# Kernel tuning notes

Measured on AMD Instinct MI355X. Metric: run time of the kernel, lower is better.

Reference implementation:

```python
import jax, jax.numpy as jnp
import numpy as np

D = 1024      # d_model
H = 16        # n_heads
HD = D // H   # head_dim = 64
B = 2
T = 2048


def setup_inputs() -> dict:
    key = jax.random.key(0)
    k0, k1, k2 = jax.random.split(key, 3)
    s = 1.0 / np.sqrt(D)
    return {
        "x": jax.random.normal(k0, (B, T, D), dtype=jnp.float32),
        "qkv_w": jax.random.normal(k1, (D, 3 * D), dtype=jnp.float32) * s,
        "qkv_b": jnp.zeros((3 * D,), dtype=jnp.float32),
        "out_w": jax.random.normal(k2, (D, D), dtype=jnp.float32) * s,
        "out_b": jnp.zeros((D,), dtype=jnp.float32),
    }


def _apply_rotary(x, rope):
    # Faithful to the torch apply_rotary: even/odd interleaved split of both
    # x and the [sin(freqs)|cos(freqs)] rope table.
    x1, x2 = x[..., ::2], x[..., 1::2]
    sin, cos = rope[..., ::2], rope[..., 1::2]
    return jnp.concatenate([x1 * cos - x2 * sin, x1 * sin + x2 * cos], axis=-1)


def reference(x, qkv_w, qkv_b, out_w, out_b):
    Bx, Tx, Dm = x.shape
    # QKV projection -> [3, B, H, T, HD]
    qkv = (x @ qkv_w + qkv_b).reshape(Bx, Tx, 3, H, HD).transpose(2, 0, 3, 1, 4)
    q, k, v = qkv[0], qkv[1], qkv[2]

    # Rotary table: rope = concat(sin(freqs), cos(freqs)) along last dim -> [T, HD]
    inv_freq = 1.0 / (10000.0 ** (jnp.arange(0, HD, 2, dtype=jnp.float32) / HD))
    t = jnp.arange(Tx, dtype=jnp.float32)
    freqs = t[:, None] * inv_freq[None, :]          # [T, HD/2]
    rope = jnp.concatenate([jnp.sin(freqs), jnp.cos(freqs)], axis=-1)  # [T, HD]

    q = _apply_rotary(q, rope)
    k = _apply_rotary(k, rope)

    scale = HD ** -0.5
    scores = jnp.einsum('bhqd,bhkd->bhqk', q, k) * scale  # [B,H,T,T]
    causal_mask = jnp.triu(jnp.ones((Tx, Tx), dtype=bool), 1)
    scores = jnp.where(causal_mask, -jnp.inf, scores)
    attn = jax.nn.softmax(scores, axis=-1)
    # dropout is identity in eval mode
    out = jnp.einsum('bhqk,bhkd->bhqd', attn, v)           # [B,H,T,HD]
    out = out.transpose(0, 2, 1, 3).reshape(Bx, Tx, Dm)    # [B,T,D]
    return out @ out_w + out_b
```

## Files before the change

### kernel.cpp

```cpp
#include <hip/hip_runtime.h>

typedef unsigned short u16;
typedef __attribute__((ext_vector_type(8))) __bf16 bf16x8;
typedef __attribute__((ext_vector_type(4))) float f32x4;

#define NB 2
#define NT 2048
#define ND 1024
#define NH 16
#define HD 64

__device__ __forceinline__ float b2f(u16 u) {
  union { float f; unsigned int i; } v; v.i = ((unsigned int)u) << 16; return v.f;
}
__device__ __forceinline__ u16 f2b(float f) {
  union { float f; unsigned int i; } v; v.f = f;
  unsigned int r = (v.i + 0x7FFFu + ((v.i >> 16) & 1u)) >> 16;
  return (u16)r;
}

__device__ __forceinline__ void gload_lds16(const u16* g, u16* lds) {
  __builtin_amdgcn_global_load_lds(
      (const __attribute__((address_space(1))) unsigned int*)(g),
      (__attribute__((address_space(3))) unsigned int*)(lds),
      16, 0, 0);
}

__device__ __forceinline__ f32x4 mfma16(bf16x8 a, bf16x8 b, f32x4 c) {
  return __builtin_amdgcn_mfma_f32_16x16x32_bf16(a, b, c, 0, 0, 0);
}

template <int N>
__device__ __forceinline__ float ror16(float x) {
  return __int_as_float(__builtin_amdgcn_update_dpp(
      __float_as_int(x), __float_as_int(x), 0x120 | N, 0xF, 0xF, true));
}
__device__ __forceinline__ float rsum16(float x) {
  x += ror16<8>(x);
  x += ror16<4>(x);
  x += ror16<2>(x);
  x += ror16<1>(x);
  return x;
}

__device__ __forceinline__ float fast_sin(float a) {
  float r = a * 0.15915494309189535f;
  r -= floorf(r);
  return __builtin_amdgcn_sinf(r);
}
__device__ __forceinline__ float fast_cos(float a) {
  float r = a * 0.15915494309189535f;
  r -= floorf(r);
  return __builtin_amdgcn_cosf(r);
}

__global__ __launch_bounds__(256) void cast_f32_bf16(const float* __restrict__ in,
                                                     u16* __restrict__ out, int n) {
  int i = (blockIdx.x * 256 + threadIdx.x) * 8;
  if (i + 8 <= n) {
#pragma unroll
    for (int j = 0; j < 8; ++j) out[i + j] = f2b(in[i + j]);
  }
}

__global__ __launch_bounds__(256) void transpose_cast(const float* __restrict__ in,
                                                      u16* __restrict__ out,
                                                      int K, int N) {
  __shared__ u16 tile[32][33];
  int n0 = blockIdx.x * 32, k0 = blockIdx.y * 32;
  int tx = threadIdx.x, ty = threadIdx.y;
  for (int i = ty; i < 32; i += 8)
    tile[i][tx] = f2b(in[(size_t)(k0 + i) * N + n0 + tx]);
  __syncthreads();
  for (int i = ty; i < 32; i += 8)
    out[(size_t)(n0 + i) * K + k0 + tx] = tile[tx][i];
}

template <int BM, bool F32OUT>
__global__ __launch_bounds__(256) void gemm_bt(const u16* __restrict__ A,
                                               const u16* __restrict__ Bt,
                                               const float* __restrict__ bias,
                                               void* __restrict__ Cv,
                                               int M, int N, int K) {
  constexpr int MI = BM / 32;
  __shared__ alignas(16) u16 As[BM * 32];
  __shared__ alignas(16) u16 Bs[128 * 32];
  const int tid = threadIdx.x;
  const int lane = tid & 63;
  const int wave = tid >> 6;
  const int l15 = lane & 15, quad = lane >> 4;
  const int wm = (wave >> 1) * (BM / 2), wn = (wave & 1) * 64;
  const int row0 = blockIdx.y * BM, col0 = blockIdx.x * 128;

  f32x4 acc[MI][4] = {};

  for (int k0 = 0; k0 < K; k0 += 32) {
    __syncthreads();
#pragma unroll
    for (int p = 0; p < BM / 64; ++p) {
      int idx8 = p * 256 + tid;
      int r = idx8 >> 2, c = (idx8 & 3) * 8;
      gload_lds16(&A[(size_t)(row0 + r) * K + k0 + c], &As[idx8 * 8]);
    }
#pragma unroll
    for (int p = 0; p < 2; ++p) {
      int idx8 = p * 256 + tid;
      int r = idx8 >> 2, c = (idx8 & 3) * 8;
      gload_lds16(&Bt[(size_t)(col0 + r) * K + k0 + c], &Bs[idx8 * 8]);
    }
    __syncthreads();
    bf16x8 af[MI], bfr[4];
#pragma unroll
    for (int mi = 0; mi < MI; ++mi)
      af[mi] = *(const bf16x8*)&As[(wm + mi * 16 + l15) * 32 + quad * 8];
#pragma unroll
    for (int ni = 0; ni < 4; ++ni)
      bfr[ni] = *(const bf16x8*)&Bs[(wn + ni * 16 + l15) * 32 + quad * 8];
#pragma unroll
    for (int mi = 0; mi < MI; ++mi)
#pragma unroll
      for (int ni = 0; ni < 4; ++ni)
        acc[mi][ni] = mfma16(af[mi], bfr[ni], acc[mi][ni]);
  }

#pragma unroll
  for (int ni = 0; ni < 4; ++ni) {
    int c = col0 + wn + ni * 16 + l15;
    float bv = bias[c];
#pragma unroll
    for (int mi = 0; mi < MI; ++mi) {
      int r0 = row0 + wm + mi * 16 + quad * 4;
      f32x4 v = acc[mi][ni];
#pragma unroll
      for (int r = 0; r < 4; ++r) {
        if (F32OUT)
          ((float*)Cv)[(size_t)(r0 + r) * N + c] = v[r] + bv;
        else
          ((u16*)Cv)[(size_t)(r0 + r) * N + c] = f2b(v[r] + bv);
      }
    }
  }
}

__global__ __launch_bounds__(256) void rope_frag(const u16* __restrict__ qkv,
                                                 u16* __restrict__ qsw,
                                                 u16* __restrict__ ksw) {
  __shared__ u16 tq[32 * 72];
  __shared__ u16 tk[32 * 72];
  const int bh = blockIdx.y;
  const int b = bh >> 4, h = bh & 15;
  const int t0 = blockIdx.x * 32;
  const int tid = threadIdx.x;

  {
    int row = tid >> 3, col = (tid & 7) * 8;
    const u16* src = &qkv[(size_t)(b * NT + t0 + row) * 3072 + h * HD + col];
    *(bf16x8*)&tq[row * 72 + col] = *(const bf16x8*)src;
    *(bf16x8*)&tk[row * 72 + col] = *(const bf16x8*)(src + ND);
  }
  __syncthreads();

  const int isK = tid >> 7;
  const int chunk = (tid >> 4) & 7;
  const int tl = tid & 15;
  const int ks = chunk >> 2, quad = chunk & 3;
  const u16* tile = isK ? tk : tq;
  u16* dst = isK ? ksw : qsw;
  const float scale = isK ? 1.0f : 0.125f;
  const float LOG1E4 = 9.210340371976184f;

#pragma unroll
  for (int rbloc = 0; rbloc < 2; ++rbloc) {
    const int row = rbloc * 16 + tl;
    const float tf = (float)(t0 + row);
    union { u16 s[8]; bf16x8 v; } o;
#pragma unroll
    for (int e = 0; e < 8; ++e) {
      int c = ks * 32 + quad * 8 + e;
      int j = c & 31;
      int c1 = 2 * j, c2 = 2 * j + 1;
      float inv1 = __expf(-((float)(c1 & 31)) * (1.0f / 32.0f) * LOG1E4);
      float inv2 = __expf(-((float)(c2 & 31)) * (1.0f / 32.0f) * LOG1E4);
      float a1 = tf * inv1, a2 = tf * inv2;
      float sA = (c1 < 32) ? fast_sin(a1) : fast_cos(a1);
      float cA = (c2 < 32) ? fast_sin(a2) : fast_cos(a2);
      float x1 = b2f(tile[row * 72 + c1]), x2 = b2f(tile[row * 72 + c2]);
      float ov = (c < 32) ? (x1 * cA - x2 * sA) : (x1 * sA + x2 * cA);
      o.s[e] = f2b(ov * scale);
    }
    size_t addr =
        ((((size_t)bh * 128 + (t0 >> 4) + rbloc) * 2 + ks) * 64 + quad * 16 + tl) * 8;
    *(bf16x8*)&dst[addr] = o.v;
  }
}

__global__ __launch_bounds__(256) void vtrans_frag(const u16* __restrict__ qkv,
                                                   u16* __restrict__ vsw) {
  __shared__ u16 tv[32 * 72];
  const int bh = blockIdx.y;
  const int b = bh >> 4, h = bh & 15;
  const int kb = blockIdx.x;
  const int tid = threadIdx.x;
  {
    int row = tid >> 3, col = (tid & 7) * 8;
    *(bf16x8*)&tv[row * 72 + col] = *(const bf16x8*)&qkv[
        (size_t)(b * NT + kb * 32 + row) * 3072 + 2 * ND + h * HD + col];
  }
  __syncthreads();
  const int ni = tid >> 6, lane = tid & 63;
  const int quad = lane >> 4, l15 = lane & 15;
  union { u16 s[8]; bf16x8 v; } o;
#pragma unroll
  for (int e = 0; e < 8; ++e)
    o.s[e] = tv[(quad * 8 + e) * 72 + ni * 16 + l15];
  *(bf16x8*)&vsw[(((size_t)bh * 64 + kb) * 4 + ni) * 512 + lane * 8] = o.v;
}

__global__ __launch_bounds__(128, 3) void flash_kernel(const u16* __restrict__ qsw,
                                                       const u16* __restrict__ ksw,
                                                       const u16* __restrict__ vsw,
                                                       u16* __restrict__ attn) {
  __shared__ alignas(16) u16 Ps[2 * 5120];
  __shared__ float Ll[32];

  const int tid = threadIdx.x;
  const int w = tid >> 6;
  const int lane = tid & 63;
  const int l15 = lane & 15, quad = lane >> 4;
  const int linear = (int)blockIdx.x;
  const int bh = linear & 31;
  const int qt = 63 - (linear >> 5);
  const int r0 = qt * 32;
  u16* Psw = &Ps[w * 5120];

  bf16x8 aq[2][2];
#pragma unroll
  for (int mi = 0; mi < 2; ++mi)
#pragma unroll
    for (int ks = 0; ks < 2; ++ks)
      aq[mi][ks] = *(const bf16x8*)&qsw[
          ((((size_t)bh * 128 + qt * 2 + mi) * 2 + ks) * 64 + lane) * 8];

  f32x4 oacc[2][4] = {};
  float lst[8] = {0.f, 0.f, 0.f, 0.f, 0.f, 0.f, 0.f, 0.f};

  const int ktmax = qt >> 2;
  for (int kt = w; kt <= ktmax; kt += 2) {
    f32x4 sacc[2][8] = {};
#pragma unroll
    for (int ks = 0; ks < 2; ++ks)
#pragma unroll
      for (int ni = 0; ni < 8; ++ni) {
        bf16x8 kf = *(const bf16x8*)&ksw[
            ((((size_t)bh * 128 + kt * 8 + ni) * 2 + ks) * 64 + lane) * 8];
        sacc[0][ni] = mfma16(aq[0][ks], kf, sacc[0][ni]);
        sacc[1][ni] = mfma16(aq[1][ks], kf, sacc[1][ni]);
      }

    const bool diag = (kt == ktmax);
    const int k0 = kt * 128;
#pragma unroll
    for (int mi = 0; mi < 2; ++mi)
#pragma unroll
      for (int r = 0; r < 4; ++r) {
        const int prow = mi * 16 + quad * 4 + r;
        float sv[8];
#pragma unroll
        for (int ni = 0; ni < 8; ++ni) sv[ni] = sacc[mi][ni][r];
        if (diag) {
#pragma unroll
          for (int ni = 0; ni < 8; ++ni)
            if (k0 + ni * 16 + l15 > r0 + prow) sv[ni] = -__builtin_inff();
        }
        float rs = 0.f;
#pragma unroll
        for (int ni = 0; ni < 8; ++ni) {
          float p = __expf(sv[ni]);
          sv[ni] = p;
          rs += p;
        }
        lst[mi * 4 + r] += rsum16(rs);
#pragma unroll
        for (int ni = 0; ni < 8; ++ni)
          Psw[(ni >> 1) * 1280 + prow * 40 + (ni & 1) * 16 + l15] = f2b(sv[ni]);
      }

    asm volatile("" ::: "memory");

#pragma unroll
    for (int ks = 0; ks < 4; ++ks) {
      bf16x8 vf[4];
#pragma unroll
      for (int ni = 0; ni < 4; ++ni)
        vf[ni] = *(const bf16x8*)&vsw[
            (((size_t)bh * 64 + kt * 4 + ks) * 4 + ni) * 512 + lane * 8];
      bf16x8 ap0 = *(const bf16x8*)&Psw[ks * 1280 + l15 * 40 + quad * 8];
      bf16x8 ap1 = *(const bf16x8*)&Psw[ks * 1280 + (16 + l15) * 40 + quad * 8];
#pragma unroll
      for (int ni = 0; ni < 4; ++ni) {
        oacc[0][ni] = mfma16(ap0, vf[ni], oacc[0][ni]);
        oacc[1][ni] = mfma16(ap1, vf[ni], oacc[1][ni]);
      }
    }
  }

  float* Of = (float*)&Ps[5120];
  if (w == 1) {
#pragma unroll
    for (int mi = 0; mi < 2; ++mi)
#pragma unroll
      for (int r = 0; r < 4; ++r) {
        const int row = mi * 16 + quad * 4 + r;
        if (l15 == 0) Ll[row] = lst[mi * 4 + r];
#pragma unroll
        for (int ni = 0; ni < 4; ++ni)
          Of[row * 64 + ni * 16 + l15] = oacc[mi][ni][r];
      }
  }
  __syncthreads();
  if (w == 0) {
    const int b = bh >> 4, h = bh & 15;
#pragma unroll
    for (int mi = 0; mi < 2; ++mi)
#pragma unroll
      for (int r = 0; r < 4; ++r) {
        const int row = mi * 16 + quad * 4 + r;
        const float rl = 1.0f / (lst[mi * 4 + r] + Ll[row]);
        const int trow = r0 + row;
#pragma unroll
        for (int ni = 0; ni < 4; ++ni) {
          float o = oacc[mi][ni][r] + Of[row * 64 + ni * 16 + l15];
          attn[((size_t)b * NT + trow) * ND + h * HD + ni * 16 + l15] = f2b(o * rl);
        }
      }
  }
}

extern "C" void kernel_launch(void* const* d_in, const int* in_sizes, int n_in,
                              void* d_out, int out_size, void* d_ws, size_t ws_size,
                              hipStream_t stream) {
  const float* x = (const float*)d_in[0];
  const float* qkv_w = (const float*)d_in[1];
  const float* qkv_b = (const float*)d_in[2];
  const float* out_w = (const float*)d_in[3];
  const float* out_b = (const float*)d_in[4];
  float* out = (float*)d_out;

  u16* ws = (u16*)d_ws;
  u16* xb    = ws;
  u16* wqkvT = xb + (size_t)4096 * 1024;
  u16* woutT = wqkvT + 3072 * 1024;
  u16* qkv   = woutT + 1024 * 1024;
  u16* qsw   = qkv + (size_t)4096 * 3072;
  u16* ksw   = qsw + (size_t)32 * 2048 * 64;
  u16* vsw   = ksw + (size_t)32 * 2048 * 64;
  u16* attn  = vsw + (size_t)32 * 2048 * 64;

  cast_f32_bf16<<<(NB * NT * ND) / (256 * 8), 256, 0, stream>>>(
      x, xb, NB * NT * ND);

  transpose_cast<<<dim3(3 * ND / 32, ND / 32), dim3(32, 8), 0, stream>>>(
      qkv_w, wqkvT, ND, 3 * ND);
  transpose_cast<<<dim3(ND / 32, ND / 32), dim3(32, 8), 0, stream>>>(
      out_w, woutT, ND, ND);

  gemm_bt<128, false><<<dim3(3 * ND / 128, NB * NT / 128), 256, 0, stream>>>(
      xb, wqkvT, qkv_b, qkv, NB * NT, 3 * ND, ND);

  rope_frag<<<dim3(NT / 32, NB * NH), 256, 0, stream>>>(qkv, qsw, ksw);
  vtrans_frag<<<dim3(NT / 32, NB * NH), 256, 0, stream>>>(qkv, vsw);

  flash_kernel<<<dim3(2048), 128, 0, stream>>>(qsw, ksw, vsw, attn);

  gemm_bt<64, true><<<dim3(ND / 128, NB * NT / 64), 256, 0, stream>>>(
      attn, woutT, out_b, out, NB * NT, ND, ND);
}
```

Baseline: 207.8 us.

## Fuse V transpose into rope prep, compute row sums via MFMA with exp2

Merges the rope and V-fragment kernels into one launch that loads Q, K and V tiles together. In the flash kernel, log2(e) is folded into the Q scale so exp2f can replace __expf. P is truncated to bf16 instead of rounded. The per-row softmax denominator is now accumulated by an extra MFMA of P against a ones vector, replacing the DPP cross-lane reductions. This trades some VALU and shuffle work for extra MFMA issue. Truncating P and summing the bf16 values slightly changes numerics.

```diff
diff --git a/kernel.cpp b/kernel.cpp
--- a/kernel.cpp
+++ b/kernel.cpp
@@ -28,19 +28,6 @@
 
 __device__ __forceinline__ f32x4 mfma16(bf16x8 a, bf16x8 b, f32x4 c) {
   return __builtin_amdgcn_mfma_f32_16x16x32_bf16(a, b, c, 0, 0, 0);
-}
-
-template <int N>
-__device__ __forceinline__ float ror16(float x) {
-  return __int_as_float(__builtin_amdgcn_update_dpp(
-      __float_as_int(x), __float_as_int(x), 0x120 | N, 0xF, 0xF, true));
-}
-__device__ __forceinline__ float rsum16(float x) {
-  x += ror16<8>(x);
-  x += ror16<4>(x);
-  x += ror16<2>(x);
-  x += ror16<1>(x);
-  return x;
 }
 
 __device__ __forceinline__ float fast_sin(float a) {
@@ -142,11 +129,13 @@
   }
 }
 
-__global__ __launch_bounds__(256) void rope_frag(const u16* __restrict__ qkv,
+__global__ __launch_bounds__(256) void prep_frag(const u16* __restrict__ qkv,
                                                  u16* __restrict__ qsw,
-                                                 u16* __restrict__ ksw) {
+                                                 u16* __restrict__ ksw,
+                                                 u16* __restrict__ vsw) {
   __shared__ u16 tq[32 * 72];
   __shared__ u16 tk[32 * 72];
+  __shared__ u16 tv[32 * 72];
   const int bh = blockIdx.y;
   const int b = bh >> 4, h = bh & 15;
   const int t0 = blockIdx.x * 32;
@@ -157,63 +146,54 @@
     const u16* src = &qkv[(size_t)(b * NT + t0 + row) * 3072 + h * HD + col];
     *(bf16x8*)&tq[row * 72 + col] = *(const bf16x8*)src;
     *(bf16x8*)&tk[row * 72 + col] = *(const bf16x8*)(src + ND);
+    *(bf16x8*)&tv[row * 72 + col] = *(const bf16x8*)(src + 2 * ND);
   }
   __syncthreads();
 
-  const int isK = tid >> 7;
-  const int chunk = (tid >> 4) & 7;
-  const int tl = tid & 15;
-  const int ks = chunk >> 2, quad = chunk & 3;
-  const u16* tile = isK ? tk : tq;
-  u16* dst = isK ? ksw : qsw;
-  const float scale = isK ? 1.0f : 0.125f;
-  const float LOG1E4 = 9.210340371976184f;
-
-#pragma unroll
-  for (int rbloc = 0; rbloc < 2; ++rbloc) {
-    const int row = rbloc * 16 + tl;
-    const float tf = (float)(t0 + row);
+  {
+    const int isK = tid >> 7;
+    const int chunk = (tid >> 4) & 7;
+    const int tl = tid & 15;
+    const int ks = chunk >> 2, quad = chunk & 3;
+    const u16* tile = isK ? tk : tq;
+    u16* dst = isK ? ksw : qsw;
+    const float scale = isK ? 1.0f : 0.18033688011112042f;
+    const float LOG1E4 = 9.210340371976184f;
+
+#pragma unroll
+    for (int rbloc = 0; rbloc < 2; ++rbloc) {
+      const int row = rbloc * 16 + tl;
+      const float tf = (float)(t0 + row);
+      union { u16 s[8]; bf16x8 v; } o;
+#pragma unroll
+      for (int e = 0; e < 8; ++e) {
+        int c = ks * 32 + quad * 8 + e;
+        int j = c & 31;
+        int c1 = 2 * j, c2 = 2 * j + 1;
+        float inv1 = __expf(-((float)(c1 & 31)) * (1.0f / 32.0f) * LOG1E4);
+        float inv2 = __expf(-((float)(c2 & 31)) * (1.0f / 32.0f) * LOG1E4);
+        float a1 = tf * inv1, a2 = tf * inv2;
+        float sA = (c1 < 32) ? fast_sin(a1) : fast_cos(a1);
+        float cA = (c2 < 32) ? fast_sin(a2) : fast_cos(a2);
+        float x1 = b2f(tile[row * 72 + c1]), x2 = b2f(tile[row * 72 + c2]);
+        float ov = (c < 32) ? (x1 * cA - x2 * sA) : (x1 * sA + x2 * cA);
+        o.s[e] = f2b(ov * scale);
+      }
+      size_t addr =
+          ((((size_t)bh * 128 + (t0 >> 4) + rbloc) * 2 + ks) * 64 + quad * 16 + tl) * 8;
+      *(bf16x8*)&dst[addr] = o.v;
+    }
+  }
+
+  {
+    const int ni = tid >> 6, lane = tid & 63;
+    const int quad = lane >> 4, l15 = lane & 15;
     union { u16 s[8]; bf16x8 v; } o;
 #pragma unroll
-    for (int e = 0; e < 8; ++e) {
-      int c = ks * 32 + quad * 8 + e;
-      int j = c & 31;
-      int c1 = 2 * j, c2 = 2 * j + 1;
-      float inv1 = __expf(-((float)(c1 & 31)) * (1.0f / 32.0f) * LOG1E4);
-      float inv2 = __expf(-((float)(c2 & 31)) * (1.0f / 32.0f) * LOG1E4);
-      float a1 = tf * inv1, a2 = tf * inv2;
-      float sA = (c1 < 32) ? fast_sin(a1) : fast_cos(a1);
-      float cA = (c2 < 32) ? fast_sin(a2) : fast_cos(a2);
-      float x1 = b2f(tile[row * 72 + c1]), x2 = b2f(tile[row * 72 + c2]);
-      float ov = (c < 32) ? (x1 * cA - x2 * sA) : (x1 * sA + x2 * cA);
-      o.s[e] = f2b(ov * scale);
-    }
-    size_t addr =
-        ((((size_t)bh * 128 + (t0 >> 4) + rbloc) * 2 + ks) * 64 + quad * 16 + tl) * 8;
-    *(bf16x8*)&dst[addr] = o.v;
-  }
-}
-
-__global__ __launch_bounds__(256) void vtrans_frag(const u16* __restrict__ qkv,
-                                                   u16* __restrict__ vsw) {
-  __shared__ u16 tv[32 * 72];
-  const int bh = blockIdx.y;
-  const int b = bh >> 4, h = bh & 15;
-  const int kb = blockIdx.x;
-  const int tid = threadIdx.x;
-  {
-    int row = tid >> 3, col = (tid & 7) * 8;
-    *(bf16x8*)&tv[row * 72 + col] = *(const bf16x8*)&qkv[
-        (size_t)(b * NT + kb * 32 + row) * 3072 + 2 * ND + h * HD + col];
-  }
-  __syncthreads();
-  const int ni = tid >> 6, lane = tid & 63;
-  const int quad = lane >> 4, l15 = lane & 15;
-  union { u16 s[8]; bf16x8 v; } o;
-#pragma unroll
-  for (int e = 0; e < 8; ++e)
-    o.s[e] = tv[(quad * 8 + e) * 72 + ni * 16 + l15];
-  *(bf16x8*)&vsw[(((size_t)bh * 64 + kb) * 4 + ni) * 512 + lane * 8] = o.v;
+    for (int e = 0; e < 8; ++e)
+      o.s[e] = tv[(quad * 8 + e) * 72 + ni * 16 + l15];
+    *(bf16x8*)&vsw[(((size_t)bh * 64 + (t0 >> 5)) * 4 + ni) * 512 + lane * 8] = o.v;
+  }
 }
 
 __global__ __launch_bounds__(128, 3) void flash_kernel(const u16* __restrict__ qsw,
@@ -233,6 +213,11 @@
   const int r0 = qt * 32;
   u16* Psw = &Ps[w * 5120];
 
+  union { u16 s[8]; bf16x8 v; } onesu;
+#pragma unroll
+  for (int e = 0; e < 8; ++e) onesu.s[e] = 0x3F80;
+  const bf16x8 ones = onesu.v;
+
   bf16x8 aq[2][2];
 #pragma unroll
   for (int mi = 0; mi < 2; ++mi)
@@ -242,7 +227,7 @@
           ((((size_t)bh * 128 + qt * 2 + mi) * 2 + ks) * 64 + lane) * 8];
 
   f32x4 oacc[2][4] = {};
-  float lst[8] = {0.f, 0.f, 0.f, 0.f, 0.f, 0.f, 0.f, 0.f};
+  f32x4 lacc[2] = {};
 
   const int ktmax = qt >> 2;
   for (int kt = w; kt <= ktmax; kt += 2) {
@@ -264,25 +249,14 @@
 #pragma unroll
       for (int r = 0; r < 4; ++r) {
         const int prow = mi * 16 + quad * 4 + r;
-        float sv[8];
-#pragma unroll
-        for (int ni = 0; ni < 8; ++ni) sv[ni] = sacc[mi][ni][r];
-        if (diag) {
-#pragma unroll
-          for (int ni = 0; ni < 8; ++ni)
-            if (k0 + ni * 16 + l15 > r0 + prow) sv[ni] = -__builtin_inff();
+#pragma unroll
+        for (int ni = 0; ni < 8; ++ni) {
+          float s = sacc[mi][ni][r];
+          if (diag && (k0 + ni * 16 + l15 > r0 + prow)) s = -__builtin_inff();
+          float p = exp2f(s);
+          Psw[(ni >> 1) * 1280 + prow * 40 + (ni & 1) * 16 + l15] =
+              (u16)(__float_as_uint(p) >> 16);
         }
-        float rs = 0.f;
-#pragma unroll
-        for (int ni = 0; ni < 8; ++ni) {
-          float p = __expf(sv[ni]);
-          sv[ni] = p;
-          rs += p;
-        }
-        lst[mi * 4 + r] += rsum16(rs);
-#pragma unroll
-        for (int ni = 0; ni < 8; ++ni)
-          Psw[(ni >> 1) * 1280 + prow * 40 + (ni & 1) * 16 + l15] = f2b(sv[ni]);
       }
 
     asm volatile("" ::: "memory");
@@ -301,6 +275,8 @@
         oacc[0][ni] = mfma16(ap0, vf[ni], oacc[0][ni]);
         oacc[1][ni] = mfma16(ap1, vf[ni], oacc[1][ni]);
       }
+      lacc[0] = mfma16(ap0, ones, lacc[0]);
+      lacc[1] = mfma16(ap1, ones, lacc[1]);
     }
   }
 
@@ -311,7 +287,7 @@
 #pragma unroll
       for (int r = 0; r < 4; ++r) {
         const int row = mi * 16 + quad * 4 + r;
-        if (l15 == 0) Ll[row] = lst[mi * 4 + r];
+        if (l15 == 0) Ll[row] = lacc[mi][r];
 #pragma unroll
         for (int ni = 0; ni < 4; ++ni)
           Of[row * 64 + ni * 16 + l15] = oacc[mi][ni][r];
@@ -325,7 +301,7 @@
 #pragma unroll
       for (int r = 0; r < 4; ++r) {
         const int row = mi * 16 + quad * 4 + r;
-        const float rl = 1.0f / (lst[mi * 4 + r] + Ll[row]);
+        const float rl = 1.0f / (lacc[mi][r] + Ll[row]);
         const int trow = r0 + row;
 #pragma unroll
         for (int ni = 0; ni < 4; ++ni) {
@@ -367,8 +343,7 @@
   gemm_bt<128, false><<<dim3(3 * ND / 128, NB * NT / 128), 256, 0, stream>>>(
       xb, wqkvT, qkv_b, qkv, NB * NT, 3 * ND, ND);
 
-  rope_frag<<<dim3(NT / 32, NB * NH), 256, 0, stream>>>(qkv, qsw, ksw);
-  vtrans_frag<<<dim3(NT / 32, NB * NH), 256, 0, stream>>>(qkv, vsw);
+  prep_frag<<<dim3(NT / 32, NB * NH), 256, 0, stream>>>(qkv, qsw, ksw, vsw);
 
   flash_kernel<<<dim3(2048), 128, 0, stream>>>(qsw, ksw, vsw, attn);
 
```

Measured after the change: 211.7 us. About the same (+1.9%).

## Fuse rope and V-transpose kernels; prefetch K/V fragments before softmax in flash loop

Applied to the files above, without the earlier changes.

Merges the rope and V fragment-transpose kernels into one launch that reads the Q, K and V tiles together, removing one kernel launch and a second pass over the qkv buffer. In the flash attention loop, all K fragments for a tile are loaded up front before the QK MFMAs, and all V fragments are issued before the softmax so their global-load latency overlaps the exp/reduction work. The cost is much higher register pressure (16+16 bf16x8 fragments live at once), which may lower occupancy under the launch bound of 3 blocks per CU or cause spills.

```diff
diff --git a/kernel.cpp b/kernel.cpp
--- a/kernel.cpp
+++ b/kernel.cpp
@@ -142,11 +142,13 @@
   }
 }
 
-__global__ __launch_bounds__(256) void rope_frag(const u16* __restrict__ qkv,
+__global__ __launch_bounds__(256) void prep_frag(const u16* __restrict__ qkv,
                                                  u16* __restrict__ qsw,
-                                                 u16* __restrict__ ksw) {
+                                                 u16* __restrict__ ksw,
+                                                 u16* __restrict__ vsw) {
   __shared__ u16 tq[32 * 72];
   __shared__ u16 tk[32 * 72];
+  __shared__ u16 tv[32 * 72];
   const int bh = blockIdx.y;
   const int b = bh >> 4, h = bh & 15;
   const int t0 = blockIdx.x * 32;
@@ -157,63 +159,54 @@
     const u16* src = &qkv[(size_t)(b * NT + t0 + row) * 3072 + h * HD + col];
     *(bf16x8*)&tq[row * 72 + col] = *(const bf16x8*)src;
     *(bf16x8*)&tk[row * 72 + col] = *(const bf16x8*)(src + ND);
+    *(bf16x8*)&tv[row * 72 + col] = *(const bf16x8*)(src + 2 * ND);
   }
   __syncthreads();
 
-  const int isK = tid >> 7;
-  const int chunk = (tid >> 4) & 7;
-  const int tl = tid & 15;
-  const int ks = chunk >> 2, quad = chunk & 3;
-  const u16* tile = isK ? tk : tq;
-  u16* dst = isK ? ksw : qsw;
-  const float scale = isK ? 1.0f : 0.125f;
-  const float LOG1E4 = 9.210340371976184f;
-
-#pragma unroll
-  for (int rbloc = 0; rbloc < 2; ++rbloc) {
-    const int row = rbloc * 16 + tl;
-    const float tf = (float)(t0 + row);
+  {
+    const int isK = tid >> 7;
+    const int chunk = (tid >> 4) & 7;
+    const int tl = tid & 15;
+    const int ks = chunk >> 2, quad = chunk & 3;
+    const u16* tile = isK ? tk : tq;
+    u16* dst = isK ? ksw : qsw;
+    const float scale = isK ? 1.0f : 0.125f;
+    const float LOG1E4 = 9.210340371976184f;
+
+#pragma unroll
+    for (int rbloc = 0; rbloc < 2; ++rbloc) {
+      const int row = rbloc * 16 + tl;
+      const float tf = (float)(t0 + row);
+      union { u16 s[8]; bf16x8 v; } o;
+#pragma unroll
+      for (int e = 0; e < 8; ++e) {
+        int c = ks * 32 + quad * 8 + e;
+        int j = c & 31;
+        int c1 = 2 * j, c2 = 2 * j + 1;
+        float inv1 = __expf(-((float)(c1 & 31)) * (1.0f / 32.0f) * LOG1E4);
+        float inv2 = __expf(-((float)(c2 & 31)) * (1.0f / 32.0f) * LOG1E4);
+        float a1 = tf * inv1, a2 = tf * inv2;
+        float sA = (c1 < 32) ? fast_sin(a1) : fast_cos(a1);
+        float cA = (c2 < 32) ? fast_sin(a2) : fast_cos(a2);
+        float x1 = b2f(tile[row * 72 + c1]), x2 = b2f(tile[row * 72 + c2]);
+        float ov = (c < 32) ? (x1 * cA - x2 * sA) : (x1 * sA + x2 * cA);
+        o.s[e] = f2b(ov * scale);
+      }
+      size_t addr =
+          ((((size_t)bh * 128 + (t0 >> 4) + rbloc) * 2 + ks) * 64 + quad * 16 + tl) * 8;
+      *(bf16x8*)&dst[addr] = o.v;
+    }
+  }
+
+  {
+    const int ni = tid >> 6, lane = tid & 63;
+    const int quad = lane >> 4, l15 = lane & 15;
     union { u16 s[8]; bf16x8 v; } o;
 #pragma unroll
-    for (int e = 0; e < 8; ++e) {
-      int c = ks * 32 + quad * 8 + e;
-      int j = c & 31;
-      int c1 = 2 * j, c2 = 2 * j + 1;
-      float inv1 = __expf(-((float)(c1 & 31)) * (1.0f / 32.0f) * LOG1E4);
-      float inv2 = __expf(-((float)(c2 & 31)) * (1.0f / 32.0f) * LOG1E4);
-      float a1 = tf * inv1, a2 = tf * inv2;
-      float sA = (c1 < 32) ? fast_sin(a1) : fast_cos(a1);
-      float cA = (c2 < 32) ? fast_sin(a2) : fast_cos(a2);
-      float x1 = b2f(tile[row * 72 + c1]), x2 = b2f(tile[row * 72 + c2]);
-      float ov = (c < 32) ? (x1 * cA - x2 * sA) : (x1 * sA + x2 * cA);
-      o.s[e] = f2b(ov * scale);
-    }
-    size_t addr =
-        ((((size_t)bh * 128 + (t0 >> 4) + rbloc) * 2 + ks) * 64 + quad * 16 + tl) * 8;
-    *(bf16x8*)&dst[addr] = o.v;
-  }
-}
-
-__global__ __launch_bounds__(256) void vtrans_frag(const u16* __restrict__ qkv,
-                                                   u16* __restrict__ vsw) {
-  __shared__ u16 tv[32 * 72];
-  const int bh = blockIdx.y;
-  const int b = bh >> 4, h = bh & 15;
-  const int kb = blockIdx.x;
-  const int tid = threadIdx.x;
-  {
-    int row = tid >> 3, col = (tid & 7) * 8;
-    *(bf16x8*)&tv[row * 72 + col] = *(const bf16x8*)&qkv[
-        (size_t)(b * NT + kb * 32 + row) * 3072 + 2 * ND + h * HD + col];
-  }
-  __syncthreads();
-  const int ni = tid >> 6, lane = tid & 63;
-  const int quad = lane >> 4, l15 = lane & 15;
-  union { u16 s[8]; bf16x8 v; } o;
-#pragma unroll
-  for (int e = 0; e < 8; ++e)
-    o.s[e] = tv[(quad * 8 + e) * 72 + ni * 16 + l15];
-  *(bf16x8*)&vsw[(((size_t)bh * 64 + kb) * 4 + ni) * 512 + lane * 8] = o.v;
+    for (int e = 0; e < 8; ++e)
+      o.s[e] = tv[(quad * 8 + e) * 72 + ni * 16 + l15];
+    *(bf16x8*)&vsw[(((size_t)bh * 64 + (t0 >> 5)) * 4 + ni) * 512 + lane * 8] = o.v;
+  }
 }
 
 __global__ __launch_bounds__(128, 3) void flash_kernel(const u16* __restrict__ qsw,
@@ -246,16 +239,30 @@
 
   const int ktmax = qt >> 2;
   for (int kt = w; kt <= ktmax; kt += 2) {
+    bf16x8 kf[2][8];
+#pragma unroll
+    for (int ks = 0; ks < 2; ++ks)
+#pragma unroll
+      for (int ni = 0; ni < 8; ++ni)
+        kf[ks][ni] = *(const bf16x8*)&ksw[
+            ((((size_t)bh * 128 + kt * 8 + ni) * 2 + ks) * 64 + lane) * 8];
+
     f32x4 sacc[2][8] = {};
 #pragma unroll
     for (int ks = 0; ks < 2; ++ks)
 #pragma unroll
       for (int ni = 0; ni < 8; ++ni) {
-        bf16x8 kf = *(const bf16x8*)&ksw[
-            ((((size_t)bh * 128 + kt * 8 + ni) * 2 + ks) * 64 + lane) * 8];
-        sacc[0][ni] = mfma16(aq[0][ks], kf, sacc[0][ni]);
-        sacc[1][ni] = mfma16(aq[1][ks], kf, sacc[1][ni]);
-      }
+        sacc[0][ni] = mfma16(aq[0][ks], kf[ks][ni], sacc[0][ni]);
+        sacc[1][ni] = mfma16(aq[1][ks], kf[ks][ni], sacc[1][ni]);
+      }
+
+    bf16x8 vf[4][4];
+#pragma unroll
+    for (int ks = 0; ks < 4; ++ks)
+#pragma unroll
+      for (int ni = 0; ni < 4; ++ni)
+        vf[ks][ni] = *(const bf16x8*)&vsw[
+            (((size_t)bh * 64 + kt * 4 + ks) * 4 + ni) * 512 + lane * 8];
 
     const bool diag = (kt == ktmax);
     const int k0 = kt * 128;
@@ -289,17 +296,12 @@
 
 #pragma unroll
     for (int ks = 0; ks < 4; ++ks) {
-      bf16x8 vf[4];
-#pragma unroll
-      for (int ni = 0; ni < 4; ++ni)
-        vf[ni] = *(const bf16x8*)&vsw[
-            (((size_t)bh * 64 + kt * 4 + ks) * 4 + ni) * 512 + lane * 8];
       bf16x8 ap0 = *(const bf16x8*)&Psw[ks * 1280 + l15 * 40 + quad * 8];
       bf16x8 ap1 = *(const bf16x8*)&Psw[ks * 1280 + (16 + l15) * 40 + quad * 8];
 #pragma unroll
       for (int ni = 0; ni < 4; ++ni) {
-        oacc[0][ni] = mfma16(ap0, vf[ni], oacc[0][ni]);
-        oacc[1][ni] = mfma16(ap1, vf[ni], oacc[1][ni]);
+        oacc[0][ni] = mfma16(ap0, vf[ks][ni], oacc[0][ni]);
+        oacc[1][ni] = mfma16(ap1, vf[ks][ni], oacc[1][ni]);
       }
     }
   }
@@ -367,8 +369,7 @@
   gemm_bt<128, false><<<dim3(3 * ND / 128, NB * NT / 128), 256, 0, stream>>>(
       xb, wqkvT, qkv_b, qkv, NB * NT, 3 * ND, ND);
 
-  rope_frag<<<dim3(NT / 32, NB * NH), 256, 0, stream>>>(qkv, qsw, ksw);
-  vtrans_frag<<<dim3(NT / 32, NB * NH), 256, 0, stream>>>(qkv, vsw);
+  prep_frag<<<dim3(NT / 32, NB * NH), 256, 0, stream>>>(qkv, qsw, ksw, vsw);
 
   flash_kernel<<<dim3(2048), 128, 0, stream>>>(qsw, ksw, vsw, attn);
 
```

Result: slower. 242.4 us (+16.6%).
